# Performance work log

Hardware: AMD Instinct MI355X
Metric: run time of the kernel (lower is better)

The kernel has to match this reference:

```python
import jax, jax.numpy as jnp
import numpy as np

N, E, D_IN, D, H = 50000, 600000, 128, 128, 128
NEG_SLOPE = 0.2  # PyG GATConv default


def setup_inputs() -> dict:
    key = jax.random.key(0)
    ks = jax.random.split(key, 10)
    s = 1.0 / np.sqrt(D)
    return {
        "x": jax.random.normal(ks[0], (N, D_IN), jnp.float32),
        "edge_index": jax.random.randint(ks[1], (2, E), 0, N, jnp.int64),
        "h": jax.random.normal(ks[2], (1, N, H), jnp.float32),
        "c": jax.random.normal(ks[3], (1, N, H), jnp.float32),
        "W": jax.random.normal(ks[4], (D_IN, D), jnp.float32) * s,
        "att_src": jax.random.normal(ks[5], (D,), jnp.float32) * s,
        "att_dst": jax.random.normal(ks[6], (D,), jnp.float32) * s,
        "bias_gat": jnp.zeros((D,), jnp.float32),
        "W_ih": jax.random.normal(ks[7], (4 * H, D), jnp.float32) * s,
        "W_hh": jax.random.normal(ks[8], (4 * H, H), jnp.float32) * s,
    }


def _gat_conv(x, edge_index, W, att_src, att_dst, bias_gat):
    n = x.shape[0]
    xs = x @ W  # [N, D]
    # add self loops (PyG default add_self_loops=True)
    loop = jnp.arange(n, dtype=edge_index.dtype)
    src = jnp.concatenate([edge_index[0], loop])
    dst = jnp.concatenate([edge_index[1], loop])
    a_src = xs @ att_src  # [N]
    a_dst = xs @ att_dst  # [N]
    e = a_src[src] + a_dst[dst]  # [E+N]
    e = jnp.where(e >= 0, e, NEG_SLOPE * e)  # leaky_relu
    # segment softmax over edges grouped by destination node
    e_max = jax.ops.segment_max(e, dst, num_segments=n)
    e_exp = jnp.exp(e - e_max[dst])
    e_sum = jax.ops.segment_sum(e_exp, dst, num_segments=n)
    alpha = e_exp / (e_sum[dst] + 1e-16)  # [E+N]
    out = jax.ops.segment_sum(alpha[:, None] * xs[src], dst, num_segments=n)
    return out + bias_gat


def _lstm_step(x, h0, c0, W_ih, W_hh):
    # torch LSTM gate order: i, f, g, o; bias=False
    gates = x @ W_ih.T + h0 @ W_hh.T  # [N, 4H]
    i, f, g, o = jnp.split(gates, 4, axis=-1)
    i, f, o = jax.nn.sigmoid(i), jax.nn.sigmoid(f), jax.nn.sigmoid(o)
    g = jnp.tanh(g)
    c1 = f * c0 + i * g
    h1 = o * jnp.tanh(c1)
    return h1, c1


def reference(x, edge_index, h, c, W, att_src, att_dst, bias_gat, W_ih, W_hh):
    xb = jnp.tanh(_gat_conv(x, edge_index, W, att_src, att_dst, bias_gat))  # [N, D]
    h1, c1 = _lstm_step(xb, h[0], c[0], W_ih, W_hh)
    # LSTM output for seq_len=1 equals the new hidden state
    return xb * 0 + h1, h1[None], c1[None]
```

## Files before the change

### kernel.cpp

```cpp
#include <hip/hip_runtime.h>
#include <hip/hip_bf16.h>
#include <math.h>

#define NEG 0.2f

typedef float f32x4 __attribute__((ext_vector_type(4)));
typedef short bf16x8 __attribute__((ext_vector_type(8)));

__device__ __forceinline__ float fsig(float x){ return 1.0f/(1.0f+__expf(-x)); }
__device__ __forceinline__ float ftanh(float x){ float e = __expf(2.0f*x); return 1.0f - 2.0f/(e+1.0f); }
__device__ __forceinline__ unsigned short f2bf(float v){
    __hip_bfloat16 b = __float2bfloat16(v);
    return *(unsigned short*)&b;
}
__device__ __forceinline__ bf16x8 pack8(float4 u, float4 v){
    bf16x8 r;
    r[0]=(short)f2bf(u.x); r[1]=(short)f2bf(u.y); r[2]=(short)f2bf(u.z); r[3]=(short)f2bf(u.w);
    r[4]=(short)f2bf(v.x); r[5]=(short)f2bf(v.y); r[6]=(short)f2bf(v.z); r[7]=(short)f2bf(v.w);
    return r;
}
__device__ __forceinline__ bf16x8 asbf(f32x4 v){ union{f32x4 f; bf16x8 h;} u; u.f=v; return u.h; }

__global__ __launch_bounds__(256) void k_pack(const float* __restrict__ W,
                                              const float* __restrict__ W_ih,
                                              const float* __restrict__ W_hh,
                                              unsigned short* __restrict__ WPX,
                                              unsigned short* __restrict__ WP2,
                                              int* __restrict__ deg, int n){
    const int bid = blockIdx.x;
    if(bid < 8){
        int f = bid*256 + threadIdx.x;
        int l = f&63, ct = (f>>6)&7, ks = f>>9;
        int k0 = ks*32 + (l>>4)*8;
        int col = ct*16 + (l&15);
        #pragma unroll
        for(int j=0;j<8;j++) WPX[(size_t)f*8+j] = f2bf(W[(size_t)(k0+j)*128 + col]);
    } else if(bid < 72){
        int f = (bid-8)*256 + threadIdx.x;
        int l = f&63, ct = (f>>6)&3, ks = (f>>8)&7, g = f>>11;
        int k0 = ks*32 + (l>>4)*8;
        int col = ct*128 + g*16 + (l&15);
        #pragma unroll
        for(int j=0;j<8;j++){
            int k = k0+j;
            float w = (k<128) ? W_ih[(size_t)col*128+k] : W_hh[(size_t)col*128+(k-128)];
            WP2[(size_t)f*8+j] = f2bf(w);
        }
    } else {
        int i = (bid-72)*256 + threadIdx.x;
        if(i < n) deg[i] = 0;
    }
}

__global__ __launch_bounds__(256,2) void k_gemm_hist(const float* __restrict__ x,
                                                     const unsigned short* __restrict__ WPX,
                                                     const float* __restrict__ att_s,
                                                     const float* __restrict__ att_d,
                                                     unsigned short* __restrict__ xsb,
                                                     float* __restrict__ a_src,
                                                     float* __restrict__ a_dst,
                                                     const int* __restrict__ ei,
                                                     int* __restrict__ deg,
                                                     int n, int ntiles, int gemmBlk,
                                                     int E, int EN){
    if((int)blockIdx.x >= gemmBlk){
        const int l = threadIdx.x & 63;
        unsigned long long m = __ballot(ei[2*l+1] != 0);
        const bool i64 = (m == 0ULL);
        int e = (blockIdx.x - gemmBlk)*256 + threadIdx.x;
        if(e>=EN) return;
        int dst = (e>=E) ? (e-E) : (i64 ? ei[2*(size_t)(E+e)] : ei[(size_t)E+e]);
        atomicAdd(&deg[dst], 1);
        return;
    }
    const int w = threadIdx.x>>6, l = threadIdx.x&63;
    const int wid = blockIdx.x*4 + w;
    const int nwaves = gemmBlk*4;
    bf16x8 B[32];
    #pragma unroll
    for(int f=0;f<32;f++) B[f] = *(const bf16x8*)(WPX + (size_t)(f*64 + l)*8);
    float asv[8], adv[8];
    #pragma unroll
    for(int ct=0;ct<8;ct++){
        asv[ct] = att_s[ct*16 + (l&15)];
        adv[ct] = att_d[ct*16 + (l&15)];
    }
    for(int rt = wid; rt < ntiles; rt += nwaves){
        int arow = rt*16 + (l&15); if(arow>=n) arow = n-1;
        const float* xr = x + (size_t)arow*128 + (l>>4)*8;
        bf16x8 A[4];
        #pragma unroll
        for(int ks=0;ks<4;ks++){
            float4 u = *(const float4*)(xr + ks*32);
            float4 v = *(const float4*)(xr + ks*32 + 4);
            A[ks] = pack8(u,v);
        }
        f32x4 acc[8];
        #pragma unroll
        for(int ct=0;ct<8;ct++) acc[ct] = (f32x4){0.f,0.f,0.f,0.f};
        #pragma unroll
        for(int ks=0;ks<4;ks++){
            #pragma unroll
            for(int ct=0;ct<8;ct++)
                acc[ct] = __builtin_amdgcn_mfma_f32_16x16x32_bf16(A[ks], B[ks*8+ct], acc[ct], 0,0,0);
        }
        #pragma unroll
        for(int reg=0;reg<4;reg++){
            int row = rt*16 + (l>>4)*4 + reg;
            float ps=0.f, pd=0.f;
            #pragma unroll
            for(int ct=0;ct<8;ct++){ ps += acc[ct][reg]*asv[ct]; pd += acc[ct][reg]*adv[ct]; }
            ps += __shfl_xor(ps,1); pd += __shfl_xor(pd,1);
            ps += __shfl_xor(ps,2); pd += __shfl_xor(pd,2);
            ps += __shfl_xor(ps,4); pd += __shfl_xor(pd,4);
            ps += __shfl_xor(ps,8); pd += __shfl_xor(pd,8);
            if((l&15)==0 && row<n){ a_src[row]=ps; a_dst[row]=pd; }
            if(row<n){
                #pragma unroll
                for(int ct=0;ct<8;ct++)
                    xsb[(size_t)row*128 + ct*16 + (l&15)] = f2bf(acc[ct][reg]);
            }
        }
    }
}

__global__ __launch_bounds__(256) void k_scan1(const int* __restrict__ deg,
                                               int* __restrict__ bsum, int n){
    __shared__ int ws[4];
    int b = blockIdx.x, t = threadIdx.x;
    int i = b*512 + t*2;
    int s = 0;
    if(i<n)   s += deg[i];
    if(i+1<n) s += deg[i+1];
    for(int off=32;off;off>>=1) s += __shfl_xor(s,off);
    if((t&63)==0) ws[t>>6]=s;
    __syncthreads();
    if(t==0) bsum[b]=ws[0]+ws[1]+ws[2]+ws[3];
}

__global__ __launch_bounds__(256) void k_scan3(const int* __restrict__ deg,
                                               const int* __restrict__ bsum,
                                               int* __restrict__ rowptr,
                                               int* __restrict__ cursor,
                                               int n, int EN){
    __shared__ int wsum[4];
    __shared__ int boff;
    int b = blockIdx.x, t = threadIdx.x;
    if(t < 64){
        int a = 0;
        for(int i=t; i<b; i+=64) a += bsum[i];
        for(int off=32;off;off>>=1) a += __shfl_xor(a,off);
        if(t==0) boff = a;
    }
    int i = b*512 + t*2;
    int d0 = (i<n)?deg[i]:0, d1 = (i+1<n)?deg[i+1]:0;
    int s = d0+d1;
    int x = s;
    int lane = t&63, wv = t>>6;
    for(int dd=1; dd<64; dd<<=1){ int y=__shfl_up(x,dd); if(lane>=dd) x+=y; }
    if(lane==63) wsum[wv]=x;
    __syncthreads();
    int woff=0;
    for(int w=0;w<wv;w++) woff += wsum[w];
    int ex = boff + woff + x - s;
    if(i<n)   { rowptr[i]  =ex;    cursor[i]  =ex;    }
    if(i+1<n) { rowptr[i+1]=ex+d0; cursor[i+1]=ex+d0; }
    if(b==0 && t==0) rowptr[n]=EN;
}

__global__ __launch_bounds__(256) void k_fill(const int* __restrict__ ei,
                                              int* __restrict__ cursor,
                                              int* __restrict__ csr_src, int E, int EN){
    const int l = threadIdx.x & 63;
    unsigned long long m = __ballot(ei[2*l+1] != 0);
    const bool i64 = (m == 0ULL);
    int e = blockIdx.x*256 + threadIdx.x;
    if(e>=EN) return;
    int src,dst;
    if(e>=E){ src=dst=e-E; }
    else if(i64){ src = ei[2*(size_t)e]; dst = ei[2*(size_t)(E+e)]; }
    else        { src = ei[(size_t)e];   dst = ei[(size_t)E+e]; }
    int pos = atomicAdd(&cursor[dst], 1);
    csr_src[pos] = src;
}

__global__ __launch_bounds__(256) void k_agg3(const int* __restrict__ rowptr,
                                              const int* __restrict__ csr_src,
                                              const float* __restrict__ a_src,
                                              const float* __restrict__ a_dst,
                                              const unsigned int* __restrict__ xsb32,
                                              const float* __restrict__ bg,
                                              const float* __restrict__ h0,
                                              unsigned short* __restrict__ xh, int n){
    const int wv = threadIdx.x>>6, l = threadIdx.x&63;
    const int dst = blockIdx.x*4 + wv;
    if(dst>=n) return;
    const int beg = rowptr[dst], end = rowptr[dst+1];
    const float ad = a_dst[dst];
    float ax=0.f, ay=0.f, psum=0.f;
    int j = beg;
    for(; j+8<=end; j+=8){
        int s0=csr_src[j],   s1=csr_src[j+1], s2=csr_src[j+2], s3=csr_src[j+3];
        int s4=csr_src[j+4], s5=csr_src[j+5], s6=csr_src[j+6], s7=csr_src[j+7];
        float e0=a_src[s0]+ad, e1=a_src[s1]+ad, e2=a_src[s2]+ad, e3=a_src[s3]+ad;
        float e4=a_src[s4]+ad, e5=a_src[s5]+ad, e6=a_src[s6]+ad, e7=a_src[s7]+ad;
        unsigned k0=xsb32[(size_t)s0*64+l], k1=xsb32[(size_t)s1*64+l];
        unsigned k2=xsb32[(size_t)s2*64+l], k3=xsb32[(size_t)s3*64+l];
        unsigned k4=xsb32[(size_t)s4*64+l], k5=xsb32[(size_t)s5*64+l];
        unsigned k6=xsb32[(size_t)s6*64+l], k7=xsb32[(size_t)s7*64+l];
        e0=e0>=0.f?e0:NEG*e0; e1=e1>=0.f?e1:NEG*e1; e2=e2>=0.f?e2:NEG*e2; e3=e3>=0.f?e3:NEG*e3;
        e4=e4>=0.f?e4:NEG*e4; e5=e5>=0.f?e5:NEG*e5; e6=e6>=0.f?e6:NEG*e6; e7=e7>=0.f?e7:NEG*e7;
        float p0=__expf(e0), p1=__expf(e1), p2=__expf(e2), p3=__expf(e3);
        float p4=__expf(e4), p5=__expf(e5), p6=__expf(e6), p7=__expf(e7);
        psum += (p0+p1+p2+p3)+(p4+p5+p6+p7);
        ax += p0*__uint_as_float(k0<<16) + p1*__uint_as_float(k1<<16)
            + p2*__uint_as_float(k2<<16) + p3*__uint_as_float(k3<<16)
            + p4*__uint_as_float(k4<<16) + p5*__uint_as_float(k5<<16)
            + p6*__uint_as_float(k6<<16) + p7*__uint_as_float(k7<<16);
        ay += p0*__uint_as_float(k0&0xffff0000u) + p1*__uint_as_float(k1&0xffff0000u)
            + p2*__uint_as_float(k2&0xffff0000u) + p3*__uint_as_float(k3&0xffff0000u)
            + p4*__uint_as_float(k4&0xffff0000u) + p5*__uint_as_float(k5&0xffff0000u)
            + p6*__uint_as_float(k6&0xffff0000u) + p7*__uint_as_float(k7&0xffff0000u);
    }
    for(; j<end; ++j){
        int s = csr_src[j];
        float sv = a_src[s]+ad;
        sv = sv>=0.f ? sv : NEG*sv;
        float p = __expf(sv);
        psum += p;
        unsigned pk = xsb32[(size_t)s*64 + l];
        ax += p*__uint_as_float(pk<<16);
        ay += p*__uint_as_float(pk & 0xffff0000u);
    }
    const float inv = 1.0f/(psum + 1e-16f);
    float t0 = ftanh(ax*inv + bg[2*l]);
    float t1 = ftanh(ay*inv + bg[2*l+1]);
    unsigned int pk = (unsigned)f2bf(t0) | ((unsigned)f2bf(t1)<<16);
    unsigned int* xr = (unsigned int*)(xh + (size_t)dst*256);
    xr[l] = pk;
    float2 hv = *(const float2*)(h0 + (size_t)dst*128 + 2*l);
    xr[64 + l] = (unsigned)f2bf(hv.x) | ((unsigned)f2bf(hv.y)<<16);
}

__global__ __launch_bounds__(256,2) void k_lstm7(const unsigned short* __restrict__ xh,
                                                 const unsigned short* __restrict__ WP2,
                                                 const float* __restrict__ c0,
                                                 float* __restrict__ out,
                                                 int n, int ntiles, int wstride){
    const int t = threadIdx.x;
    const int w = t>>6, l = t&63;
    const int wid = blockIdx.x*4 + w;
    const int g = wid & 7, wgi = wid >> 3;
    const unsigned short* wp = WP2 + (size_t)g*16384;
    f32x4 B[32];
    #pragma unroll
    for(int f=0;f<32;f++) B[f] = *(const f32x4*)(wp + (size_t)(f*64 + l)*8);
    #pragma unroll
    for(int f=0;f<32;f++) asm volatile("" : "+v"(B[f]));
    const size_t nn = (size_t)n*128;
    const int col = g*16 + (l&15);
    int rt = wgi;
    if(rt >= ntiles) return;
    bf16x8 A[8]; float cc[4];
    {
        int arow = rt*16 + (l&15); if(arow>=n) arow=n-1;
        const unsigned short* ar = xh + (size_t)arow*256 + (l>>4)*8;
        #pragma unroll
        for(int ks=0;ks<8;ks++) A[ks] = *(const bf16x8*)(ar + ks*32);
        int rbase = rt*16 + (l>>4)*4;
        #pragma unroll
        for(int r=0;r<4;r++){ int rr=rbase+r; if(rr>=n) rr=n-1; cc[r]=c0[(size_t)rr*128+col]; }
    }
    while(rt < ntiles){
        const int rtn = rt + wstride;
        bf16x8 A2[8]; float cc2[4];
        if(rtn < ntiles){
            int arow = rtn*16 + (l&15); if(arow>=n) arow=n-1;
            const unsigned short* ar = xh + (size_t)arow*256 + (l>>4)*8;
            #pragma unroll
            for(int ks=0;ks<8;ks++) A2[ks] = *(const bf16x8*)(ar + ks*32);
            int rbase = rtn*16 + (l>>4)*4;
            #pragma unroll
            for(int r=0;r<4;r++){ int rr=rbase+r; if(rr>=n) rr=n-1; cc2[r]=c0[(size_t)rr*128+col]; }
        }
        f32x4 acc[4];
        #pragma unroll
        for(int ct=0;ct<4;ct++) acc[ct] = (f32x4){0.f,0.f,0.f,0.f};
        #pragma unroll
        for(int ks=0;ks<8;ks++){
            #pragma unroll
            for(int ct=0;ct<4;ct++)
                acc[ct] = __builtin_amdgcn_mfma_f32_16x16x32_bf16(A[ks], asbf(B[ks*4+ct]), acc[ct], 0,0,0);
        }
        #pragma unroll
        for(int reg=0;reg<4;reg++){
            int row = rt*16 + (l>>4)*4 + reg;
            if(row>=n) continue;
            float gi=acc[0][reg], gf=acc[1][reg], gg=acc[2][reg], go=acc[3][reg];
            float c1v = fsig(gf)*cc[reg] + fsig(gi)*ftanh(gg);
            float h1v = fsig(go)*ftanh(c1v);
            out[(size_t)row*128+col]        = h1v;
            out[nn + (size_t)row*128+col]   = h1v;
            out[2*nn + (size_t)row*128+col] = c1v;
        }
        rt = rtn;
        if(rt < ntiles){
            #pragma unroll
            for(int ks=0;ks<8;ks++) A[ks] = A2[ks];
            #pragma unroll
            for(int r=0;r<4;r++) cc[r] = cc2[r];
        }
    }
}

extern "C" void kernel_launch(void* const* d_in, const int* in_sizes, int n_in,
                              void* d_out, int out_size, void* d_ws, size_t ws_size,
                              hipStream_t stream) {
    const float* x      = (const float*)d_in[0];
    const int*   ei     = (const int*)  d_in[1];
    const float* h      = (const float*)d_in[2];
    const float* c      = (const float*)d_in[3];
    const float* W      = (const float*)d_in[4];
    const float* atts   = (const float*)d_in[5];
    const float* attd   = (const float*)d_in[6];
    const float* bias   = (const float*)d_in[7];
    const float* W_ih   = (const float*)d_in[8];
    const float* W_hh   = (const float*)d_in[9];
    float* out = (float*)d_out;

    const int n  = in_sizes[0]/128;
    const int E  = in_sizes[1]/2;
    const int EN = E + n;
    const int NB = (n + 511)/512;
    const int ntiles = (n + 15)/16;
    const int n2 = ntiles*16;
    const int histBlk = (EN + 255)/256;
    const int degBlk  = (n + 255)/256;

    unsigned short* xsb = (unsigned short*)d_ws;
    unsigned short* xh  = xsb + (size_t)n*128;
    unsigned short* WP2 = xh + (size_t)n2*256;
    unsigned short* WPX = WP2 + 131072;
    float* a_src = (float*)(WPX + 16384);
    float* a_dst = a_src + n;
    int*   deg    = (int*)(a_dst + n);
    int*   rowptr = deg + n;
    int*   cursor = rowptr + n + 1;
    int*   bsum   = cursor + n;
    int*   csr_src= bsum + 128;

    k_pack<<<72+degBlk,256,0,stream>>>(W, W_ih, W_hh, WPX, WP2, deg, n);
    k_gemm_hist<<<1024+histBlk,256,0,stream>>>(x, WPX, atts, attd, xsb, a_src, a_dst,
                                               ei, deg, n, ntiles, 1024, E, EN);
    k_scan1<<<NB,256,0,stream>>>(deg,bsum,n);
    k_scan3<<<NB,256,0,stream>>>(deg,bsum,rowptr,cursor,n,EN);
    k_fill<<<histBlk,256,0,stream>>>(ei,cursor,csr_src,E,EN);
    k_agg3<<<(n+3)/4,256,0,stream>>>(rowptr,csr_src,a_src,a_dst,(const unsigned int*)xsb,bias,h,xh,n);
    k_lstm7<<<1024,256,0,stream>>>(xh, WP2, c, out, n, ntiles, 512);
}
```

Before: 167.0 us.

## Split LSTM gate GEMM into 16 column groups with half the register-resident weights

```diff
diff --git a/kernel.cpp b/kernel.cpp
--- a/kernel.cpp
+++ b/kernel.cpp
@@ -37,9 +37,12 @@
         for(int j=0;j<8;j++) WPX[(size_t)f*8+j] = f2bf(W[(size_t)(k0+j)*128 + col]);
     } else if(bid < 72){
         int f = (bid-8)*256 + threadIdx.x;
-        int l = f&63, ct = (f>>6)&3, ks = (f>>8)&7, g = f>>11;
+        int l = f&63, q = (f>>6)&15, g = f>>10;
+        int ks = q>>1, ct = q&1;
         int k0 = ks*32 + (l>>4)*8;
-        int col = ct*128 + g*16 + (l&15);
+        int sub = l&15;
+        int gate = ct*2 + (sub>>3);
+        int col = gate*128 + g*8 + (sub&7);
         #pragma unroll
         for(int j=0;j<8;j++){
             int k = k0+j;
@@ -242,73 +245,57 @@
     xr[64 + l] = (unsigned)f2bf(hv.x) | ((unsigned)f2bf(hv.y)<<16);
 }
 
-__global__ __launch_bounds__(256,2) void k_lstm7(const unsigned short* __restrict__ xh,
-                                                 const unsigned short* __restrict__ WP2,
-                                                 const float* __restrict__ c0,
-                                                 float* __restrict__ out,
-                                                 int n, int ntiles, int wstride){
+__global__ __launch_bounds__(256,4) void k_lstm12(const unsigned short* __restrict__ xh,
+                                                  const unsigned short* __restrict__ WP2,
+                                                  const float* __restrict__ c0,
+                                                  float* __restrict__ out,
+                                                  int n, int ntiles, int wstride){
     const int t = threadIdx.x;
     const int w = t>>6, l = t&63;
     const int wid = blockIdx.x*4 + w;
-    const int g = wid & 7, wgi = wid >> 3;
-    const unsigned short* wp = WP2 + (size_t)g*16384;
-    f32x4 B[32];
+    const int g = wid & 15, wgi = wid >> 4;
+    const unsigned short* wp = WP2 + (size_t)g*8192;
+    f32x4 B[16];
     #pragma unroll
-    for(int f=0;f<32;f++) B[f] = *(const f32x4*)(wp + (size_t)(f*64 + l)*8);
+    for(int q=0;q<16;q++) B[q] = *(const f32x4*)(wp + (size_t)(q*64 + l)*8);
     #pragma unroll
-    for(int f=0;f<32;f++) asm volatile("" : "+v"(B[f]));
+    for(int q=0;q<16;q++) asm volatile("" : "+v"(B[q]));
     const size_t nn = (size_t)n*128;
-    const int col = g*16 + (l&15);
-    int rt = wgi;
-    if(rt >= ntiles) return;
-    bf16x8 A[8]; float cc[4];
-    {
+    const bool lower = ((l&15) < 8);
+    const int col = g*8 + (l&7);
+    for(int rt = wgi; rt < ntiles; rt += wstride){
         int arow = rt*16 + (l&15); if(arow>=n) arow=n-1;
         const unsigned short* ar = xh + (size_t)arow*256 + (l>>4)*8;
+        bf16x8 A[8];
         #pragma unroll
         for(int ks=0;ks<8;ks++) A[ks] = *(const bf16x8*)(ar + ks*32);
-        int rbase = rt*16 + (l>>4)*4;
-        #pragma unroll
-        for(int r=0;r<4;r++){ int rr=rbase+r; if(rr>=n) rr=n-1; cc[r]=c0[(size_t)rr*128+col]; }
-    }
-    while(rt < ntiles){
-        const int rtn = rt + wstride;
-        bf16x8 A2[8]; float cc2[4];
-        if(rtn < ntiles){
-            int arow = rtn*16 + (l&15); if(arow>=n) arow=n-1;
-            const unsigned short* ar = xh + (size_t)arow*256 + (l>>4)*8;
+        const int rbase = rt*16 + (l>>4)*4;
+        float cc[4];
+        if(lower){
             #pragma unroll
-            for(int ks=0;ks<8;ks++) A2[ks] = *(const bf16x8*)(ar + ks*32);
-            int rbase = rtn*16 + (l>>4)*4;
-            #pragma unroll
-            for(int r=0;r<4;r++){ int rr=rbase+r; if(rr>=n) rr=n-1; cc2[r]=c0[(size_t)rr*128+col]; }
-        }
-        f32x4 acc[4];
-        #pragma unroll
-        for(int ct=0;ct<4;ct++) acc[ct] = (f32x4){0.f,0.f,0.f,0.f};
+            for(int r=0;r<4;r++){ int rr=rbase+r; if(rr>=n) rr=n-1; cc[r]=c0[(size_t)rr*128+col]; }
+        }
+        f32x4 acc0 = (f32x4){0.f,0.f,0.f,0.f};
+        f32x4 acc1 = (f32x4){0.f,0.f,0.f,0.f};
         #pragma unroll
         for(int ks=0;ks<8;ks++){
-            #pragma unroll
-            for(int ct=0;ct<4;ct++)
-                acc[ct] = __builtin_amdgcn_mfma_f32_16x16x32_bf16(A[ks], asbf(B[ks*4+ct]), acc[ct], 0,0,0);
+            acc0 = __builtin_amdgcn_mfma_f32_16x16x32_bf16(A[ks], asbf(B[ks*2  ]), acc0, 0,0,0);
+            acc1 = __builtin_amdgcn_mfma_f32_16x16x32_bf16(A[ks], asbf(B[ks*2+1]), acc1, 0,0,0);
         }
         #pragma unroll
         for(int reg=0;reg<4;reg++){
-            int row = rt*16 + (l>>4)*4 + reg;
-            if(row>=n) continue;
-            float gi=acc[0][reg], gf=acc[1][reg], gg=acc[2][reg], go=acc[3][reg];
-            float c1v = fsig(gf)*cc[reg] + fsig(gi)*ftanh(gg);
-            float h1v = fsig(go)*ftanh(c1v);
-            out[(size_t)row*128+col]        = h1v;
-            out[nn + (size_t)row*128+col]   = h1v;
-            out[2*nn + (size_t)row*128+col] = c1v;
-        }
-        rt = rtn;
-        if(rt < ntiles){
-            #pragma unroll
-            for(int ks=0;ks<8;ks++) A[ks] = A2[ks];
-            #pragma unroll
-            for(int r=0;r<4;r++) cc[r] = cc2[r];
+            int row = rbase + reg;
+            float v0 = acc0[reg];
+            float v1 = acc1[reg];
+            float p0 = __shfl_xor(v0, 8);
+            float p1 = __shfl_xor(v1, 8);
+            if(lower && row<n){
+                float c1v = fsig(p0)*cc[reg] + fsig(v0)*ftanh(v1);
+                float h1v = fsig(p1)*ftanh(c1v);
+                out[(size_t)row*128+col]        = h1v;
+                out[nn + (size_t)row*128+col]   = h1v;
+                out[2*nn + (size_t)row*128+col] = c1v;
+            }
         }
     }
 }
@@ -356,5 +343,5 @@
     k_scan3<<<NB,256,0,stream>>>(deg,bsum,rowptr,cursor,n,EN);
     k_fill<<<histBlk,256,0,stream>>>(ei,cursor,csr_src,E,EN);
     k_agg3<<<(n+3)/4,256,0,stream>>>(rowptr,csr_src,a_src,a_dst,(const unsigned int*)xsb,bias,h,xh,n);
-    k_lstm7<<<1024,256,0,stream>>>(xh, WP2, c, out, n, ntiles, 512);
-}
+    k_lstm12<<<1024,256,0,stream>>>(xh, WP2, c, out, n, ntiles, 256);
+}
```

Result: slower. 187.1 us (+12.0%).
